# Kernel optimization log

Measured on AMD Instinct MI355X. Metric: run time of the kernel, lower is better.

The kernel has to match this reference:

```python
import math
import jax, jax.numpy as jnp
import numpy as np

B, L, D_IN, H, NLAYER, FUT, MDIM = 16, 128, 8, 128, 2, 12, 2

def setup_inputs() -> dict:
    key = jax.random.key(0)
    ks = jax.random.split(key, 16)
    def rn(k, shape, scale=0.05):
        return jax.random.normal(k, shape, jnp.float32) * scale
    return {
        'history': jax.random.normal(ks[0], (B, L, D_IN), jnp.float32),
        'history_mask': jnp.ones((B, L), jnp.float32),
        'Wp': rn(ks[1], (D_IN, H)), 'bp': jnp.zeros((H,), jnp.float32),
        'We1': rn(ks[2], (NLAYER, 4, H)), 'be1': jnp.zeros((NLAYER, H), jnp.float32),
        'We2': rn(ks[3], (NLAYER, H, H)), 'be2': jnp.zeros((NLAYER, H), jnp.float32),
        'Wa1': rn(ks[4], (NLAYER, 3 * H, H)), 'ba1': jnp.zeros((NLAYER, H), jnp.float32),
        'wa2': rn(ks[5], (NLAYER, H)), 'ba2': jnp.zeros((NLAYER,), jnp.float32),
        'Wm1': rn(ks[6], (NLAYER, 2 * H, H)), 'bm1': jnp.zeros((NLAYER, H), jnp.float32),
        'Wm2': rn(ks[7], (NLAYER, H, H)), 'bm2': jnp.zeros((NLAYER, H), jnp.float32),
        'Wo1': rn(ks[8], (NLAYER, 2 * H, H)), 'bo1': jnp.zeros((NLAYER, H), jnp.float32),
        'Wo2': rn(ks[9], (NLAYER, H, H)), 'bo2': jnp.zeros((NLAYER, H), jnp.float32),
        'ln_g': jnp.ones((NLAYER, H), jnp.float32), 'ln_b': jnp.zeros((NLAYER, H), jnp.float32),
        'hg': jnp.ones((D_IN + H,), jnp.float32), 'hb': jnp.zeros((D_IN + H,), jnp.float32),
        'Wh1': rn(ks[10], (D_IN + H, H)), 'bh1': jnp.zeros((H,), jnp.float32),
        'Wh2': rn(ks[11], (H, FUT * MDIM)), 'bh2': jnp.zeros((FUT * MDIM,), jnp.float32),
    }

def _layer_norm(x, g, b):
    mu = jnp.mean(x, -1, keepdims=True)
    var = jnp.mean((x - mu) ** 2, -1, keepdims=True)
    return (x - mu) * jax.lax.rsqrt(var + 1e-5) * g + b

def _forward(history, history_mask, Wp, bp, We1, be1, We2, be2, Wa1, ba1, wa2, ba2,
             Wm1, bm1, Wm2, bm2, Wo1, bo1, Wo2, bo2, ln_g, ln_b, hg, hb, Wh1, bh1, Wh2, bh2):
    valid = history_mask > 0
    vm = valid.astype(jnp.float32)[..., None]
    ts = jnp.cumsum(jnp.maximum(history[..., 5], 0.0), axis=1)
    # edge features [B,L,L,4]: dist, dt/300, same_src, same_step
    lat, lon, src_flag = history[..., 0], history[..., 1], history[..., 6]
    dlat = lat[:, :, None] - lat[:, None, :]
    dlon = lon[:, :, None] - lon[:, None, :]
    dist = jnp.sqrt(dlat * dlat + dlon * dlon + 1e-8)
    dt = jnp.abs(ts[:, :, None] - ts[:, None, :]) / 300.0
    same_src = (src_flag[:, :, None] == src_flag[:, None, :]).astype(jnp.float32)
    same_step = jnp.broadcast_to(jnp.eye(L, dtype=jnp.float32), (B, L, L))
    edge_feat = jnp.stack([dist, dt, same_src, same_step], axis=-1)
    h = (history @ Wp + bp) * vm
    inv = 1.0 / math.sqrt(H)
    for l in range(NLAYER):
        eh = jax.nn.relu(edge_feat @ We1[l] + be1[l]) @ We2[l] + be2[l]  # [B,L,L,H]
        # att MLP on concat([src,dst,edge]) -> split first weight into blocks
        sa = h @ Wa1[l, :H]       # src term, varies over i
        da = h @ Wa1[l, H:2 * H]  # dst term, varies over j
        att_hid = jnp.tanh(sa[:, :, None, :] + da[:, None, :, :] + eh @ Wa1[l, 2 * H:] + ba1[l])
        att = (att_hid @ wa2[l] + ba2[l]) * inv  # [B,L,L]
        att = jnp.where(valid[:, None, :], att, -1e9)  # key invalid
        att = jnp.where(valid[:, :, None], att, -1e9)  # query invalid
        w = jax.nn.softmax(att, axis=-1)
        # msg MLP on concat([src, edge])
        msg = jax.nn.relu((h @ Wm1[l, :H])[:, :, None, :] + eh @ Wm1[l, H:] + bm1[l]) @ Wm2[l] + bm2[l]
        agg = jnp.einsum('bij,bijk->bik', w, msg)
        out = jax.nn.relu(h @ Wo1[l, :H] + agg @ Wo1[l, H:] + bo1[l]) @ Wo2[l] + bo2[l]
        h = _layer_norm(h + out, ln_g[l], ln_b[l]) * vm
    # decoder state: last valid step
    vc = jnp.clip(jnp.sum(history_mask, axis=1).astype(jnp.int32), 1, L)
    last = vc - 1
    bidx = jnp.arange(B)
    ds = jnp.concatenate([history[bidx, last], h[bidx, last]], axis=-1)
    x = _layer_norm(ds, hg, hb)
    pred = (jax.nn.relu(x @ Wh1 + bh1) @ Wh2 + bh2).reshape(B, FUT, MDIM)
    pred = jnp.nan_to_num(pred, nan=0.0, posinf=1e4, neginf=-1e4)
    return pred, h

def reference(history, history_mask, Wp, bp, We1, be1, We2, be2, Wa1, ba1, wa2, ba2,
              Wm1, bm1, Wm2, bm2, Wo1, bo1, Wo2, bo2, ln_g, ln_b, hg, hb, Wh1, bh1, Wh2, bh2):
    return _forward(history, history_mask, Wp, bp, We1, be1, We2, be2, Wa1, ba1, wa2, ba2,
                    Wm1, bm1, Wm2, bm2, Wo1, bo1, Wo2, bo2, ln_g, ln_b, hg, hb, Wh1, bh1, Wh2, bh2)
```

## Files before the change

### kernel.cpp

```cpp
#include <hip/hip_runtime.h>
#include <math.h>

#define BB 16
#define LL 128
#define D_IN 8
#define HH 128
#define NLAYER 2
#define FUT 12
#define MDIM 2

typedef __attribute__((ext_vector_type(8))) __bf16 bf16x8;
typedef __attribute__((ext_vector_type(8))) short short8v;
typedef __attribute__((ext_vector_type(4))) float f32x4;

#define MFMA_B16(A, B, C) __builtin_amdgcn_mfma_f32_16x16x32_bf16(A, B, C, 0, 0, 0)

static __device__ __forceinline__ short f2bf(float f) {
    union { float f; unsigned u; } v; v.f = f;
    unsigned r = v.u + 0x7FFFu + ((v.u >> 16) & 1u);
    return (short)(r >> 16);
}

static __device__ __forceinline__ float tanh_fast(float x) {
    float e = __expf(2.f * x);
    return 1.f - 2.f / (e + 1.f);
}

__global__ __launch_bounds__(256) void k_prep(const float* __restrict__ hist, const float* __restrict__ mask,
                                              const float* __restrict__ Wp, const float* __restrict__ bp,
                                              const float* __restrict__ We2, const float* __restrict__ be2,
                                              const float* __restrict__ Wa1, const float* __restrict__ ba1,
                                              const float* __restrict__ Wm1, const float* __restrict__ bm1,
                                              const float* __restrict__ Wo1, const float* __restrict__ Wm2,
                                              const float* __restrict__ Wo2,
                                              float* __restrict__ ts, float* __restrict__ h,
                                              short* __restrict__ AmT, short* __restrict__ MmT,
                                              float* __restrict__ ca, float* __restrict__ cm,
                                              short* __restrict__ WT4, short* __restrict__ WT3) {
    __shared__ float row[HH];
    __shared__ float pa[256], pm[256];
    const int bid = blockIdx.x, tid = threadIdx.x;
    const int NC = NLAYER * (HH + 1);
    if (bid < BB) {
        int b = bid;
        if (tid < LL) row[tid] = fmaxf(hist[(b * LL + tid) * D_IN + 5], 0.f);
        __syncthreads();
        for (int d = 1; d < LL; d <<= 1) {
            float add = (tid < LL && tid >= d) ? row[tid - d] : 0.f;
            __syncthreads();
            if (tid < LL) row[tid] += add;
            __syncthreads();
        }
        if (tid < LL) ts[b * LL + tid] = row[tid];
        int k = tid & (HH - 1);
        float wp_r[D_IN];
#pragma unroll
        for (int f = 0; f < D_IN; f++) wp_r[f] = Wp[f * HH + k];
        float bpk = bp[k];
        int jbase = tid >> 7;
        for (int e = 0; e < 64; e++) {
            int j = e * 2 + jbase;
            int bj = b * LL + j;
            const float* hr = hist + (size_t)bj * D_IN;
            float acc = bpk;
#pragma unroll
            for (int f = 0; f < D_IN; f++) acc += hr[f] * wp_r[f];
            h[(size_t)bj * HH + k] = acc * (mask[bj] > 0.f ? 1.f : 0.f);
        }
    } else if (bid < BB + NC) {
        int cb = bid - BB;
        int l = cb / (HH + 1);
        int p = cb % (HH + 1);
        const float* WaE = Wa1 + (size_t)(l * 3 * HH + 2 * HH) * HH;
        const float* WmE = Wm1 + (size_t)(l * 2 * HH + HH) * HH;
        int q = tid & 127, kh = tid >> 7;
        if (tid < HH) row[tid] = (p < HH) ? We2[(size_t)(l * HH + p) * HH + tid] : be2[l * HH + tid];
        __syncthreads();
        float a = 0.f, m = 0.f;
        int kbase = kh * 64;
        for (int k = 0; k < 64; k++) {
            float w = row[kbase + k];
            a += w * WaE[(size_t)(kbase + k) * HH + q];
            m += w * WmE[(size_t)(kbase + k) * HH + q];
        }
        pa[tid] = a;
        pm[tid] = m;
        __syncthreads();
        if (tid < HH) {
            a = pa[tid] + pa[128 + tid];
            m = pm[tid] + pm[128 + tid];
            if (p < HH) {
                AmT[(size_t)l * HH * HH + tid * HH + p] = f2bf(a);
                MmT[(size_t)l * HH * HH + tid * HH + p] = f2bf(m);
            } else {
                ca[l * HH + tid] = a + ba1[l * HH + tid];
                cm[l * HH + tid] = m + bm1[l * HH + tid];
            }
        }
    } else {
        int m7 = bid - BB - NC;
        int l = m7 / 7, m = m7 % 7;
        const float* src;
        switch (m) {
            case 0: src = Wa1 + (size_t)(l * 3 * HH) * HH; break;
            case 1: src = Wa1 + (size_t)(l * 3 * HH + HH) * HH; break;
            case 2: src = Wm1 + (size_t)(l * 2 * HH) * HH; break;
            case 3: src = Wo1 + (size_t)(l * 2 * HH) * HH; break;
            case 4: src = Wm2 + (size_t)l * HH * HH; break;
            case 5: src = Wo1 + (size_t)(l * 2 * HH + HH) * HH; break;
            default: src = Wo2 + (size_t)l * HH * HH; break;
        }
        short* dst = (m < 4) ? (WT4 + (size_t)(l * 4 + m) * HH * HH)
                             : (WT3 + (size_t)(l * 3 + (m - 4)) * HH * HH);
#pragma unroll 4
        for (int e = 0; e < 64; e++) {
            int idx = e * 256 + tid;
            int c = idx >> 7, kk = idx & (HH - 1);
            dst[c * HH + kk] = f2bf(src[kk * HH + c]);
        }
    }
}

__global__ __launch_bounds__(256) void k_pre(const float* __restrict__ h, const short* __restrict__ WT4,
                                             const float* __restrict__ ca, const float* __restrict__ cm,
                                             float* __restrict__ base_a, float* __restrict__ da,
                                             float* __restrict__ base_m, float* __restrict__ oa, int l) {
    __shared__ __align__(16) short hA[16][136];
    const int tid = threadIdx.x, lane = tid & 63, wv = tid >> 6;
    const int lo = lane & 15, g4 = lane >> 4;
    const int rt = blockIdx.x >> 1, half = blockIdx.x & 1;
    const int r0 = rt * 16;
    {
        int row = tid >> 4, cc = (tid & 15) * 8;
        const float* hr = h + (size_t)(r0 + row) * HH + cc;
        short8v pk;
#pragma unroll
        for (int e = 0; e < 8; e++) pk[e] = f2bf(hr[e]);
        *(short8v*)&hA[row][cc] = pk;
    }
    __syncthreads();
    bf16x8 af[4];
#pragma unroll
    for (int ks = 0; ks < 4; ks++)
        af[ks] = *(const bf16x8*)&hA[lo][ks * 32 + g4 * 8];
    const int mat = half * 2 + (wv & 1);
    const int ctbase = (wv >> 1) * 4;
    const short* Wl = WT4 + (size_t)(l * 4 + mat) * HH * HH;
    float* dst;
    const float* bias = nullptr;
    if (mat == 0) { dst = base_a; bias = ca + l * HH; }
    else if (mat == 1) dst = da;
    else if (mat == 2) { dst = base_m; bias = cm + l * HH; }
    else dst = oa;
#pragma unroll
    for (int cc2 = 0; cc2 < 4; cc2++) {
        int col = (ctbase + cc2) * 16 + lo;
        bf16x8 Bf[4];
#pragma unroll
        for (int ks = 0; ks < 4; ks++)
            Bf[ks] = *(const bf16x8*)(Wl + (size_t)col * HH + ks * 32 + g4 * 8);
        f32x4 acc = (f32x4){0.f, 0.f, 0.f, 0.f};
#pragma unroll
        for (int ks = 0; ks < 4; ks++) acc = MFMA_B16(af[ks], Bf[ks], acc);
        float bv = bias ? bias[col] : 0.f;
#pragma unroll
        for (int rg = 0; rg < 4; rg++)
            dst[(size_t)(r0 + g4 * 4 + rg) * HH + col] = acc[rg] + bv;
    }
}

__global__ __launch_bounds__(512) void k_attn(
    const float* __restrict__ hist, const float* __restrict__ mask, const float* __restrict__ ts,
    const float* __restrict__ base_a_g, const float* __restrict__ base_m_g, const float* __restrict__ da,
    const short* __restrict__ AmT, const short* __restrict__ MmT,
    const float* __restrict__ wa2, const float* __restrict__ ba2,
    const float* __restrict__ We1, const float* __restrict__ be1,
    float* __restrict__ v_out, int l) {
    __shared__ __align__(16) short t_lds[LL][LL];
    __shared__ __align__(16) float bufA[1024];
    __shared__ float w_lds[LL];
    __shared__ float val_s[LL];

    const int tid = threadIdx.x;
    const int lane = tid & 63;
    const int wv = tid >> 6;
    const int lo = lane & 15, g4 = lane >> 4;
    const int k0 = wv * 16 + lo;
    const int bi = blockIdx.x, b = bi >> 7, i = bi & (LL - 1);

    const float base_a_r = base_a_g[(size_t)bi * HH + k0];
    const float base_m_r = base_m_g[(size_t)bi * HH + k0];
    const float wa2_r = wa2[l * HH + k0];
    const float ba2l = ba2[l];

    bf16x8 Bf[4];
#pragma unroll
    for (int ks = 0; ks < 4; ks++)
        Bf[ks] = *(const bf16x8*)(AmT + (size_t)l * HH * HH + (size_t)k0 * HH + ks * 32 + g4 * 8);

    bufA[tid] = We1[l * 4 * HH + tid];
    if (tid < LL) {
        val_s[tid] = mask[b * LL + tid];
        bufA[512 + tid] = be1[l * HH + tid];
    }
    __syncthreads();

    {
        int jj = tid & (LL - 1);
        int q4 = tid >> 7;
        const float* hri = hist + (size_t)(b * LL + i) * D_IN;
        const float* hrj = hist + (size_t)(b * LL + jj) * D_IN;
        float dlat = hri[0] - hrj[0], dlon = hri[1] - hrj[1];
        float ea = sqrtf(dlat * dlat + dlon * dlon + 1e-8f);
        float eb = fabsf(ts[b * LL + i] - ts[b * LL + jj]) * (1.f / 300.f);
        float ec = (hri[6] == hrj[6]) ? 1.f : 0.f;
        float ed = (jj == i) ? 1.f : 0.f;
        char* trow = (char*)t_lds + jj * 256;
        int swz = (jj & 7) << 4;
#pragma unroll
        for (int pass = 0; pass < 4; pass++) {
            int r0c = (q4 + pass * 4) * 8;
            short8v pk;
#pragma unroll
            for (int hv = 0; hv < 2; hv++) {
                f32x4 wa = *(const f32x4*)&bufA[r0c + hv * 4];
                f32x4 wb = *(const f32x4*)&bufA[128 + r0c + hv * 4];
                f32x4 wc = *(const f32x4*)&bufA[256 + r0c + hv * 4];
                f32x4 wd = *(const f32x4*)&bufA[384 + r0c + hv * 4];
                f32x4 wbe = *(const f32x4*)&bufA[512 + r0c + hv * 4];
#pragma unroll
                for (int e = 0; e < 4; e++) {
                    float v = ea * wa[e] + eb * wb[e] + ec * wc[e] + ed * wd[e] + wbe[e];
                    pk[hv * 4 + e] = f2bf(fmaxf(v, 0.f));
                }
            }
            *(short8v*)(trow + ((r0c * 2) ^ swz)) = pk;
        }
    }
    __syncthreads();

    const float* da_b = da + (size_t)(b * LL) * HH;
    const int rswz = (lo & 7) << 4;

#pragma unroll
    for (int jh = 0; jh < 2; jh++) {
        f32x4 acc[4];
#pragma unroll
        for (int m = 0; m < 4; m++)
#pragma unroll
            for (int rg = 0; rg < 4; rg++)
                acc[m][rg] = da_b[(size_t)((jh * 4 + m) * 16 + g4 * 4 + rg) * HH + k0];
#pragma unroll
        for (int ks = 0; ks < 4; ks++) {
            bf16x8 tf[4];
#pragma unroll
            for (int m = 0; m < 4; m++) {
                int row = (jh * 4 + m) * 16 + lo;
                tf[m] = *(const bf16x8*)((const char*)t_lds + row * 256 + ((ks * 64 + g4 * 16) ^ rswz));
            }
#pragma unroll
            for (int m = 0; m < 4; m++) acc[m] = MFMA_B16(tf[m], Bf[ks], acc[m]);
        }
#pragma unroll
        for (int m = 0; m < 4; m++)
#pragma unroll
            for (int rg = 0; rg < 4; rg++) {
                float p = tanh_fast(acc[m][rg] + base_a_r) * wa2_r;
                p += __shfl_xor(p, 1);
                p += __shfl_xor(p, 2);
                p += __shfl_xor(p, 4);
                p += __shfl_xor(p, 8);
                if (lo == 0) bufA[wv * LL + (jh * 4 + m) * 16 + g4 * 4 + rg] = p;
            }
    }

#pragma unroll
    for (int ks = 0; ks < 4; ks++)
        Bf[ks] = *(const bf16x8*)(MmT + (size_t)l * HH * HH + (size_t)k0 * HH + ks * 32 + g4 * 8);
    __syncthreads();

    {
        const float inv = 0.08838834764831845f;
        float vi = val_s[i];
        float a0 = ba2l, a1 = ba2l;
#pragma unroll
        for (int w = 0; w < 8; w++) {
            a0 += bufA[w * LL + lane];
            a1 += bufA[w * LL + 64 + lane];
        }
        a0 *= inv; a1 *= inv;
        if (!(val_s[lane] > 0.f) || !(vi > 0.f)) a0 = -1e9f;
        if (!(val_s[64 + lane] > 0.f) || !(vi > 0.f)) a1 = -1e9f;
        float m = fmaxf(a0, a1);
#pragma unroll
        for (int d = 1; d < 64; d <<= 1) m = fmaxf(m, __shfl_xor(m, d));
        float e0 = __expf(a0 - m), e1 = __expf(a1 - m);
        float s = e0 + e1;
#pragma unroll
        for (int d = 1; d < 64; d <<= 1) s += __shfl_xor(s, d);
        float rs = 1.f / s;
        w_lds[lane] = e0 * rs;
        w_lds[64 + lane] = e1 * rs;
    }

    float mac = 0.f;
#pragma unroll
    for (int jh = 0; jh < 2; jh++) {
        f32x4 acc[4];
#pragma unroll
        for (int m = 0; m < 4; m++) acc[m] = (f32x4){0.f, 0.f, 0.f, 0.f};
#pragma unroll
        for (int ks = 0; ks < 4; ks++) {
            bf16x8 tf[4];
#pragma unroll
            for (int m = 0; m < 4; m++) {
                int row = (jh * 4 + m) * 16 + lo;
                tf[m] = *(const bf16x8*)((const char*)t_lds + row * 256 + ((ks * 64 + g4 * 16) ^ rswz));
            }
#pragma unroll
            for (int m = 0; m < 4; m++) acc[m] = MFMA_B16(tf[m], Bf[ks], acc[m]);
        }
#pragma unroll
        for (int m = 0; m < 4; m++) {
            f32x4 wj4 = *(const f32x4*)&w_lds[(jh * 4 + m) * 16 + g4 * 4];
#pragma unroll
            for (int rg = 0; rg < 4; rg++)
                mac += wj4[rg] * fmaxf(acc[m][rg] + base_m_r, 0.f);
        }
    }
    mac += __shfl_xor(mac, 16);
    mac += __shfl_xor(mac, 32);
    if (g4 == 0) v_out[(size_t)bi * HH + k0] = mac;
}

__global__ __launch_bounds__(256) void k_post(
    const float* __restrict__ v, const float* __restrict__ oa_in, const float* __restrict__ h,
    const float* __restrict__ mask, const short* __restrict__ WT3,
    const float* __restrict__ bm2, const float* __restrict__ bo1, const float* __restrict__ bo2,
    const float* __restrict__ ln_g, const float* __restrict__ ln_b,
    float* __restrict__ hout, float* __restrict__ hcopy, int l,
    int do_pre, const short* __restrict__ WT4, const float* __restrict__ ca, const float* __restrict__ cm,
    float* __restrict__ base_a, float* __restrict__ da, float* __restrict__ base_m, float* __restrict__ oa_out,
    const float* __restrict__ hist, const float* __restrict__ hg, const float* __restrict__ hb,
    const float* __restrict__ Wh1, const float* __restrict__ bh1,
    const float* __restrict__ Wh2, const float* __restrict__ bh2, float* __restrict__ dec_out) {
    __shared__ __align__(16) short xA[16][136];
    __shared__ __align__(16) short iA[16][136];
    __shared__ float red[2][4][16];
    __shared__ float ln_row[HH];
    __shared__ float dec_x[D_IN + HH];
    const int tid = threadIdx.x, lane = tid & 63, wv = tid >> 6;
    const int lo = lane & 15, g4 = lane >> 4;
    const int r0 = blockIdx.x * 16;

    float oaR[2][4], hR[2][4], vmR[4];
    float bm2R[2], bo1R[2], bo2R[2], gR[2], bR[2];
#pragma unroll
    for (int ct = 0; ct < 2; ct++) {
        int c = wv * 32 + ct * 16 + lo;
        bm2R[ct] = bm2[l * HH + c];
        bo1R[ct] = bo1[l * HH + c];
        bo2R[ct] = bo2[l * HH + c];
        gR[ct] = ln_g[l * HH + c];
        bR[ct] = ln_b[l * HH + c];
    }
#pragma unroll
    for (int rg = 0; rg < 4; rg++) {
        int r = r0 + g4 * 4 + rg;
        vmR[rg] = mask[r];
#pragma unroll
        for (int ct = 0; ct < 2; ct++) {
            int c = wv * 32 + ct * 16 + lo;
            oaR[ct][rg] = oa_in[(size_t)r * HH + c];
            hR[ct][rg] = h[(size_t)r * HH + c];
        }
    }

    int lastRow = -1;
    if (hcopy) {
        float mv = (tid < LL) ? mask[(r0 >> 7) * LL + tid] : 0.f;
#pragma unroll
        for (int d = 1; d < 64; d <<= 1) mv += __shfl_xor(mv, d);
        if (lane == 0) red[0][wv][0] = mv;
    }

    {
        int row = tid >> 4, cc = (tid & 15) * 8;
        const float* vr = v + (size_t)(r0 + row) * HH + cc;
        short8v pk;
#pragma unroll
        for (int e = 0; e < 8; e++) pk[e] = f2bf(vr[e]);
        *(short8v*)&xA[row][cc] = pk;
    }
    __syncthreads();

    if (hcopy) {
        int vc = (int)(red[0][0][0] + red[0][1][0] + red[0][2][0] + red[0][3][0]);
        vc = min(max(vc, 1), LL);
        lastRow = (r0 & ~(LL - 1)) + vc - 1;
    }

    bf16x8 af[4], Bf[2][4];
    f32x4 acc[2];

    {
        const short* W = WT3 + (size_t)(l * 3 + 0) * HH * HH;
#pragma unroll
        for (int ks = 0; ks < 4; ks++) af[ks] = *(const bf16x8*)&xA[lo][ks * 32 + g4 * 8];
#pragma unroll
        for (int ct = 0; ct < 2; ct++) {
            int col = wv * 32 + ct * 16 + lo;
#pragma unroll
            for (int ks = 0; ks < 4; ks++)
                Bf[ct][ks] = *(const bf16x8*)(W + (size_t)col * HH + ks * 32 + g4 * 8);
        }
        acc[0] = (f32x4){0.f, 0.f, 0.f, 0.f};
        acc[1] = (f32x4){0.f, 0.f, 0.f, 0.f};
#pragma unroll
        for (int ks = 0; ks < 4; ks++) {
            acc[0] = MFMA_B16(af[ks], Bf[0][ks], acc[0]);
            acc[1] = MFMA_B16(af[ks], Bf[1][ks], acc[1]);
        }
#pragma unroll
        for (int ct = 0; ct < 2; ct++)
#pragma unroll
            for (int rg = 0; rg < 4; rg++)
                iA[g4 * 4 + rg][wv * 32 + ct * 16 + lo] = f2bf(acc[ct][rg] + bm2R[ct]);
    }
    __syncthreads();

    {
        const short* W = WT3 + (size_t)(l * 3 + 1) * HH * HH;
#pragma unroll
        for (int ks = 0; ks < 4; ks++) af[ks] = *(const bf16x8*)&iA[lo][ks * 32 + g4 * 8];
#pragma unroll
        for (int ct = 0; ct < 2; ct++) {
            int col = wv * 32 + ct * 16 + lo;
#pragma unroll
            for (int ks = 0; ks < 4; ks++)
                Bf[ct][ks] = *(const bf16x8*)(W + (size_t)col * HH + ks * 32 + g4 * 8);
        }
        acc[0] = (f32x4){0.f, 0.f, 0.f, 0.f};
        acc[1] = (f32x4){0.f, 0.f, 0.f, 0.f};
#pragma unroll
        for (int ks = 0; ks < 4; ks++) {
            acc[0] = MFMA_B16(af[ks], Bf[0][ks], acc[0]);
            acc[1] = MFMA_B16(af[ks], Bf[1][ks], acc[1]);
        }
        __syncthreads();
#pragma unroll
        for (int ct = 0; ct < 2; ct++)
#pragma unroll
            for (int rg = 0; rg < 4; rg++)
                xA[g4 * 4 + rg][wv * 32 + ct * 16 + lo] =
                    f2bf(fmaxf(acc[ct][rg] + oaR[ct][rg] + bo1R[ct], 0.f));
    }
    __syncthreads();

    float y[2][4];
    {
        const short* W = WT3 + (size_t)(l * 3 + 2) * HH * HH;
#pragma unroll
        for (int ks = 0; ks < 4; ks++) af[ks] = *(const bf16x8*)&xA[lo][ks * 32 + g4 * 8];
#pragma unroll
        for (int ct = 0; ct < 2; ct++) {
            int col = wv * 32 + ct * 16 + lo;
#pragma unroll
            for (int ks = 0; ks < 4; ks++)
                Bf[ct][ks] = *(const bf16x8*)(W + (size_t)col * HH + ks * 32 + g4 * 8);
        }
        acc[0] = (f32x4){0.f, 0.f, 0.f, 0.f};
        acc[1] = (f32x4){0.f, 0.f, 0.f, 0.f};
#pragma unroll
        for (int ks = 0; ks < 4; ks++) {
            acc[0] = MFMA_B16(af[ks], Bf[0][ks], acc[0]);
            acc[1] = MFMA_B16(af[ks], Bf[1][ks], acc[1]);
        }
#pragma unroll
        for (int ct = 0; ct < 2; ct++)
#pragma unroll
            for (int rg = 0; rg < 4; rg++)
                y[ct][rg] = acc[ct][rg] + bo2R[ct] + hR[ct][rg];
    }
#pragma unroll
    for (int rg = 0; rg < 4; rg++) {
        float s = y[0][rg] + y[1][rg];
        float s2 = y[0][rg] * y[0][rg] + y[1][rg] * y[1][rg];
#pragma unroll
        for (int d = 1; d < 16; d <<= 1) { s += __shfl_xor(s, d); s2 += __shfl_xor(s2, d); }
        if (lo == 0) {
            red[0][wv][g4 * 4 + rg] = s;
            red[1][wv][g4 * 4 + rg] = s2;
        }
    }
    __syncthreads();
#pragma unroll
    for (int rg = 0; rg < 4; rg++) {
        int rl = g4 * 4 + rg;
        float mu = (red[0][0][rl] + red[0][1][rl] + red[0][2][rl] + red[0][3][rl]) * (1.f / HH);
        float ex2 = (red[1][0][rl] + red[1][1][rl] + red[1][2][rl] + red[1][3][rl]) * (1.f / HH);
        float var = ex2 - mu * mu;
        float rs = rsqrtf(var + 1e-5f);
        float vm = vmR[rg] > 0.f ? 1.f : 0.f;
        int r = r0 + rl;
#pragma unroll
        for (int ct = 0; ct < 2; ct++) {
            int c = wv * 32 + ct * 16 + lo;
            float hv = ((y[ct][rg] - mu) * rs * gR[ct] + bR[ct]) * vm;
            hout[(size_t)r * HH + c] = hv;
            if (hcopy) hcopy[(size_t)r * HH + c] = hv;
            if (do_pre) xA[rl][c] = f2bf(hv);
            if (lastRow >= 0 && r == lastRow) ln_row[c] = hv;
        }
    }

    if (do_pre) {
        __syncthreads();
        bf16x8 af2[4];
#pragma unroll
        for (int ks = 0; ks < 4; ks++) af2[ks] = *(const bf16x8*)&xA[lo][ks * 32 + g4 * 8];
        int ln = l + 1;
        const short* Wl = WT4 + (size_t)(ln * 4 + wv) * HH * HH;
        float* dst;
        const float* bias = nullptr;
        if (wv == 0) { dst = base_a; bias = ca + ln * HH; }
        else if (wv == 1) dst = da;
        else if (wv == 2) { dst = base_m; bias = cm + ln * HH; }
        else dst = oa_out;
#pragma unroll
        for (int ct = 0; ct < 8; ct++) {
            int col = ct * 16 + lo;
            bf16x8 Bf2[4];
#pragma unroll
            for (int ks = 0; ks < 4; ks++)
                Bf2[ks] = *(const bf16x8*)(Wl + (size_t)col * HH + ks * 32 + g4 * 8);
            f32x4 a2 = (f32x4){0.f, 0.f, 0.f, 0.f};
#pragma unroll
            for (int ks = 0; ks < 4; ks++) a2 = MFMA_B16(af2[ks], Bf2[ks], a2);
            float bv = bias ? bias[col] : 0.f;
#pragma unroll
            for (int rg = 0; rg < 4; rg++)
                dst[(size_t)(r0 + g4 * 4 + rg) * HH + col] = a2[rg] + bv;
        }
    }

    if (hcopy && lastRow >= r0 && lastRow < r0 + 16) {
        const int N = D_IN + HH;
        __syncthreads();
        if (tid < D_IN) dec_x[tid] = hist[(size_t)lastRow * D_IN + tid];
        if (tid < HH) dec_x[D_IN + tid] = ln_row[tid];
        __syncthreads();
        float px = (tid < N) ? dec_x[tid] : 0.f;
        float px2 = px * px;
#pragma unroll
        for (int d = 1; d < 64; d <<= 1) { px += __shfl_xor(px, d); px2 += __shfl_xor(px2, d); }
        if (lane == 0) { red[0][wv][0] = px; red[1][wv][0] = px2; }
        __syncthreads();
        float mu = (red[0][0][0] + red[0][1][0] + red[0][2][0] + red[0][3][0]) / (float)N;
        float ex2 = (red[1][0][0] + red[1][1][0] + red[1][2][0] + red[1][3][0]) / (float)N;
        float var = ex2 - mu * mu;
        float rs = rsqrtf(var + 1e-5f);
        if (tid < N) dec_x[tid] = (dec_x[tid] - mu) * rs * hg[tid] + hb[tid];
        __syncthreads();
        if (tid < HH) {
            float a = bh1[tid];
            for (int f = 0; f < N; f++) a += dec_x[f] * Wh1[(size_t)f * HH + tid];
            ln_row[tid] = fmaxf(a, 0.f);
        }
        __syncthreads();
        if (tid < FUT * MDIM) {
            float o = bh2[tid];
            for (int k = 0; k < HH; k++) o += ln_row[k] * Wh2[(size_t)k * FUT * MDIM + tid];
            if (isnan(o)) o = 0.f;
            else if (isinf(o)) o = (o > 0.f) ? 1e4f : -1e4f;
            dec_out[(r0 >> 7) * FUT * MDIM + tid] = o;
        }
    }
}

extern "C" void kernel_launch(void* const* d_in, const int* in_sizes, int n_in,
                              void* d_out, int out_size, void* d_ws, size_t ws_size,
                              hipStream_t stream) {
    const float* hist = (const float*)d_in[0];
    const float* mask = (const float*)d_in[1];
    const float* Wp  = (const float*)d_in[2];
    const float* bp  = (const float*)d_in[3];
    const float* We1 = (const float*)d_in[4];
    const float* be1 = (const float*)d_in[5];
    const float* We2 = (const float*)d_in[6];
    const float* be2 = (const float*)d_in[7];
    const float* Wa1 = (const float*)d_in[8];
    const float* ba1 = (const float*)d_in[9];
    const float* wa2 = (const float*)d_in[10];
    const float* ba2 = (const float*)d_in[11];
    const float* Wm1 = (const float*)d_in[12];
    const float* bm1 = (const float*)d_in[13];
    const float* Wm2 = (const float*)d_in[14];
    const float* bm2 = (const float*)d_in[15];
    const float* Wo1 = (const float*)d_in[16];
    const float* bo1 = (const float*)d_in[17];
    const float* Wo2 = (const float*)d_in[18];
    const float* bo2 = (const float*)d_in[19];
    const float* ln_g = (const float*)d_in[20];
    const float* ln_b = (const float*)d_in[21];
    const float* hg  = (const float*)d_in[22];
    const float* hb  = (const float*)d_in[23];
    const float* Wh1 = (const float*)d_in[24];
    const float* bh1 = (const float*)d_in[25];
    const float* Wh2 = (const float*)d_in[26];
    const float* bh2 = (const float*)d_in[27];
    float* out = (float*)d_out;

    float* ws = (float*)d_ws;
    float* ts_w   = ws; ws += BB * LL;
    float* h_w    = ws; ws += BB * LL * HH;
    float* da_w   = ws; ws += BB * LL * HH;
    float* ba_w   = ws; ws += BB * LL * HH;
    float* bm_w   = ws; ws += BB * LL * HH;
    float* oa_w   = ws; ws += BB * LL * HH;
    float* v_w    = ws; ws += BB * LL * HH;
    float* ca_w   = ws; ws += NLAYER * HH;
    float* cm_w   = ws; ws += NLAYER * HH;
    short* AmT_w  = (short*)ws; ws += NLAYER * HH * HH / 2;
    short* MmT_w  = (short*)ws; ws += NLAYER * HH * HH / 2;
    short* WT4_w  = (short*)ws; ws += NLAYER * 4 * HH * HH / 2;
    short* WT3_w  = (short*)ws; ws += NLAYER * 3 * HH * HH / 2;

    const int NPREP = BB + NLAYER * (HH + 1) + NLAYER * 7;
    k_prep<<<NPREP, 256, 0, stream>>>(hist, mask, Wp, bp, We2, be2, Wa1, ba1, Wm1, bm1,
                                      Wo1, Wm2, Wo2, ts_w, h_w, AmT_w, MmT_w, ca_w, cm_w, WT4_w, WT3_w);
    k_pre<<<BB * LL / 16 * 2, 256, 0, stream>>>(h_w, WT4_w, ca_w, cm_w, ba_w, da_w, bm_w, oa_w, 0);
    for (int l = 0; l < NLAYER; l++) {
        k_attn<<<BB * LL, 512, 0, stream>>>(hist, mask, ts_w, ba_w, bm_w, da_w, AmT_w, MmT_w,
                                            wa2, ba2, We1, be1, v_w, l);
        int do_pre = (l < NLAYER - 1) ? 1 : 0;
        float* hcopy = (l == NLAYER - 1) ? (out + BB * FUT * MDIM) : nullptr;
        k_post<<<BB * LL / 16, 256, 0, stream>>>(v_w, oa_w, h_w, mask, WT3_w, bm2, bo1, bo2,
                                                 ln_g, ln_b, h_w, hcopy, l,
                                                 do_pre, WT4_w, ca_w, cm_w, ba_w, da_w, bm_w, oa_w,
                                                 hist, hg, hb, Wh1, bh1, Wh2, bh2, out);
    }
}
```

Baseline: 268.4 us.

## Swap MFMA operand order in attention kernel to cut cross-lane reductions

Swaps the A/B operands of the MFMA in both attention matmuls so each lane holds four consecutive hidden channels for one neighbour j, instead of four neighbours for one channel. This lets the per-channel bias, tanh-weighting and initial accumulator loads become vectorized float4 reads, and the attention-score reduction drops from four shuffle steps per element to two per group of four. The edge-feature build folds the same-source and bias terms into a selected base row and adds the self-loop term only on the diagonal, which removes multiplies. The precompute loop also gains an unroll pragma. The message-side reduction now needs four vectors of shuffles, which offsets part of the saving.

Result: faster. 253.4 us (-5.6%).

```diff
diff --git a/kernel.cpp b/kernel.cpp
--- a/kernel.cpp
+++ b/kernel.cpp
@@ -78,6 +78,7 @@
         __syncthreads();
         float a = 0.f, m = 0.f;
         int kbase = kh * 64;
+#pragma unroll 4
         for (int k = 0; k < 64; k++) {
             float w = row[kbase + k];
             a += w * WaE[(size_t)(kbase + k) * HH + q];
@@ -185,23 +186,29 @@
     const int lane = tid & 63;
     const int wv = tid >> 6;
     const int lo = lane & 15, g4 = lane >> 4;
-    const int k0 = wv * 16 + lo;
+    const int kq = wv * 16 + g4 * 4;
     const int bi = blockIdx.x, b = bi >> 7, i = bi & (LL - 1);
 
-    const float base_a_r = base_a_g[(size_t)bi * HH + k0];
-    const float base_m_r = base_m_g[(size_t)bi * HH + k0];
-    const float wa2_r = wa2[l * HH + k0];
+    const f32x4 ba4 = *(const f32x4*)(base_a_g + (size_t)bi * HH + kq);
+    const f32x4 bm4 = *(const f32x4*)(base_m_g + (size_t)bi * HH + kq);
+    const f32x4 wa4 = *(const f32x4*)(wa2 + l * HH + kq);
     const float ba2l = ba2[l];
 
     bf16x8 Bf[4];
 #pragma unroll
     for (int ks = 0; ks < 4; ks++)
-        Bf[ks] = *(const bf16x8*)(AmT + (size_t)l * HH * HH + (size_t)k0 * HH + ks * 32 + g4 * 8);
-
-    bufA[tid] = We1[l * 4 * HH + tid];
-    if (tid < LL) {
-        val_s[tid] = mask[b * LL + tid];
-        bufA[512 + tid] = be1[l * HH + tid];
+        Bf[ks] = *(const bf16x8*)(AmT + (size_t)l * HH * HH + (size_t)(wv * 16 + lo) * HH + ks * 32 + g4 * 8);
+
+    {
+        const float* We1l = We1 + l * 4 * HH;
+        const float* be1l = be1 + l * HH;
+        if (tid < 256) bufA[tid] = We1l[tid];
+        else if (tid < 384) bufA[tid] = be1l[tid - 256];
+        else bufA[tid] = be1l[tid - 384] + We1l[256 + (tid - 384)];
+        if (tid < 128) {
+            bufA[512 + tid] = We1l[384 + tid];
+            val_s[tid] = mask[b * LL + tid];
+        }
     }
     __syncthreads();
 
@@ -213,27 +220,29 @@
         float dlat = hri[0] - hrj[0], dlon = hri[1] - hrj[1];
         float ea = sqrtf(dlat * dlat + dlon * dlon + 1e-8f);
         float eb = fabsf(ts[b * LL + i] - ts[b * LL + jj]) * (1.f / 300.f);
-        float ec = (hri[6] == hrj[6]) ? 1.f : 0.f;
-        float ed = (jj == i) ? 1.f : 0.f;
+        const float* basep = bufA + ((hri[6] == hrj[6]) ? 384 : 256);
         char* trow = (char*)t_lds + jj * 256;
         int swz = (jj & 7) << 4;
 #pragma unroll
         for (int pass = 0; pass < 4; pass++) {
             int r0c = (q4 + pass * 4) * 8;
-            short8v pk;
+            float vv[8];
 #pragma unroll
             for (int hv = 0; hv < 2; hv++) {
                 f32x4 wa = *(const f32x4*)&bufA[r0c + hv * 4];
                 f32x4 wb = *(const f32x4*)&bufA[128 + r0c + hv * 4];
-                f32x4 wc = *(const f32x4*)&bufA[256 + r0c + hv * 4];
-                f32x4 wd = *(const f32x4*)&bufA[384 + r0c + hv * 4];
-                f32x4 wbe = *(const f32x4*)&bufA[512 + r0c + hv * 4];
-#pragma unroll
-                for (int e = 0; e < 4; e++) {
-                    float v = ea * wa[e] + eb * wb[e] + ec * wc[e] + ed * wd[e] + wbe[e];
-                    pk[hv * 4 + e] = f2bf(fmaxf(v, 0.f));
-                }
+                f32x4 bs = *(const f32x4*)&basep[r0c + hv * 4];
+#pragma unroll
+                for (int e = 0; e < 4; e++)
+                    vv[hv * 4 + e] = ea * wa[e] + eb * wb[e] + bs[e];
             }
+            if (jj == i) {
+#pragma unroll
+                for (int e = 0; e < 8; e++) vv[e] += bufA[512 + r0c + e];
+            }
+            short8v pk;
+#pragma unroll
+            for (int e = 0; e < 8; e++) pk[e] = f2bf(fmaxf(vv[e], 0.f));
             *(short8v*)(trow + ((r0c * 2) ^ swz)) = pk;
         }
     }
@@ -246,10 +255,10 @@
     for (int jh = 0; jh < 2; jh++) {
         f32x4 acc[4];
 #pragma unroll
-        for (int m = 0; m < 4; m++)
-#pragma unroll
-            for (int rg = 0; rg < 4; rg++)
-                acc[m][rg] = da_b[(size_t)((jh * 4 + m) * 16 + g4 * 4 + rg) * HH + k0];
+        for (int m = 0; m < 4; m++) {
+            int j0 = (jh * 4 + m) * 16 + lo;
+            acc[m] = *(const f32x4*)(da_b + (size_t)j0 * HH + kq);
+        }
 #pragma unroll
         for (int ks = 0; ks < 4; ks++) {
             bf16x8 tf[4];
@@ -259,24 +268,24 @@
                 tf[m] = *(const bf16x8*)((const char*)t_lds + row * 256 + ((ks * 64 + g4 * 16) ^ rswz));
             }
 #pragma unroll
-            for (int m = 0; m < 4; m++) acc[m] = MFMA_B16(tf[m], Bf[ks], acc[m]);
-        }
-#pragma unroll
-        for (int m = 0; m < 4; m++)
-#pragma unroll
-            for (int rg = 0; rg < 4; rg++) {
-                float p = tanh_fast(acc[m][rg] + base_a_r) * wa2_r;
-                p += __shfl_xor(p, 1);
-                p += __shfl_xor(p, 2);
-                p += __shfl_xor(p, 4);
-                p += __shfl_xor(p, 8);
-                if (lo == 0) bufA[wv * LL + (jh * 4 + m) * 16 + g4 * 4 + rg] = p;
-            }
+            for (int m = 0; m < 4; m++) acc[m] = MFMA_B16(Bf[ks], tf[m], acc[m]);
+        }
+#pragma unroll
+        for (int m = 0; m < 4; m++) {
+            float p0 = tanh_fast(acc[m][0] + ba4[0]) * wa4[0];
+            float p1 = tanh_fast(acc[m][1] + ba4[1]) * wa4[1];
+            float p2 = tanh_fast(acc[m][2] + ba4[2]) * wa4[2];
+            float p3 = tanh_fast(acc[m][3] + ba4[3]) * wa4[3];
+            float p = (p0 + p1) + (p2 + p3);
+            p += __shfl_xor(p, 16);
+            p += __shfl_xor(p, 32);
+            if (g4 == 0) bufA[wv * LL + (jh * 4 + m) * 16 + lo] = p;
+        }
     }
 
 #pragma unroll
     for (int ks = 0; ks < 4; ks++)
-        Bf[ks] = *(const bf16x8*)(MmT + (size_t)l * HH * HH + (size_t)k0 * HH + ks * 32 + g4 * 8);
+        Bf[ks] = *(const bf16x8*)(MmT + (size_t)l * HH * HH + (size_t)(wv * 16 + lo) * HH + ks * 32 + g4 * 8);
     __syncthreads();
 
     {
@@ -303,7 +312,7 @@
         w_lds[64 + lane] = e1 * rs;
     }
 
-    float mac = 0.f;
+    f32x4 macv = (f32x4){0.f, 0.f, 0.f, 0.f};
 #pragma unroll
     for (int jh = 0; jh < 2; jh++) {
         f32x4 acc[4];
@@ -318,19 +327,24 @@
                 tf[m] = *(const bf16x8*)((const char*)t_lds + row * 256 + ((ks * 64 + g4 * 16) ^ rswz));
             }
 #pragma unroll
-            for (int m = 0; m < 4; m++) acc[m] = MFMA_B16(tf[m], Bf[ks], acc[m]);
+            for (int m = 0; m < 4; m++) acc[m] = MFMA_B16(Bf[ks], tf[m], acc[m]);
         }
 #pragma unroll
         for (int m = 0; m < 4; m++) {
-            f32x4 wj4 = *(const f32x4*)&w_lds[(jh * 4 + m) * 16 + g4 * 4];
+            float wj = w_lds[(jh * 4 + m) * 16 + lo];
 #pragma unroll
             for (int rg = 0; rg < 4; rg++)
-                mac += wj4[rg] * fmaxf(acc[m][rg] + base_m_r, 0.f);
-        }
-    }
-    mac += __shfl_xor(mac, 16);
-    mac += __shfl_xor(mac, 32);
-    if (g4 == 0) v_out[(size_t)bi * HH + k0] = mac;
+                macv[rg] += wj * fmaxf(acc[m][rg] + bm4[rg], 0.f);
+        }
+    }
+#pragma unroll
+    for (int rg = 0; rg < 4; rg++) {
+        macv[rg] += __shfl_xor(macv[rg], 1);
+        macv[rg] += __shfl_xor(macv[rg], 2);
+        macv[rg] += __shfl_xor(macv[rg], 4);
+        macv[rg] += __shfl_xor(macv[rg], 8);
+    }
+    if (lo == 0) *(f32x4*)(v_out + (size_t)bi * HH + kq) = macv;
 }
 
 __global__ __launch_bounds__(256) void k_post(
```
